# Performance work log

Hardware: AMD Instinct MI355X
Metric: run time of the kernel (lower is better)

Reference implementation:

```python
import jax, jax.numpy as jnp
import numpy as np

D = 1024
N = 16
H = D // N  # 64
F = 4096
LOG2E = 1.442695041


def _rms_norm(x, scale, eps=1e-6):
    var = jnp.mean(x * x, axis=-1, keepdims=True)
    return x * jax.lax.rsqrt(var + eps) * scale


def _layer_norm(x, gamma, beta, eps=1e-5):
    m = jnp.mean(x, axis=-1, keepdims=True)
    v = jnp.mean(jnp.square(x - m), axis=-1, keepdims=True)
    return (x - m) * jax.lax.rsqrt(v + eps) * gamma + beta


def setup_inputs() -> dict:
    key = jax.random.key(0)
    ks = jax.random.split(key, 12)
    B, T = 8, 1024
    s = 0.02
    return {
        "x": jax.random.normal(ks[0], (B, T, D), dtype=jnp.float32),
        "padding": jnp.ones((B, T), dtype=jnp.float32),
        "rms_scale": jnp.ones((D,), dtype=jnp.float32),
        "per_dim_scale": jnp.zeros((H,), dtype=jnp.float32),
        "wq": jax.random.normal(ks[1], (D, N, H), dtype=jnp.float32) * s,
        "bq": jnp.zeros((N, H), dtype=jnp.float32),
        "wk": jax.random.normal(ks[2], (D, N, H), dtype=jnp.float32) * s,
        "bk": jnp.zeros((N, H), dtype=jnp.float32),
        "wv": jax.random.normal(ks[3], (D, N, H), dtype=jnp.float32) * s,
        "bv": jnp.zeros((N, H), dtype=jnp.float32),
        "wo": jax.random.normal(ks[4], (D, N, H), dtype=jnp.float32) * s,
        "bo": jnp.zeros((D,), dtype=jnp.float32),
        "ln_gamma": jnp.ones((D,), dtype=jnp.float32),
        "ln_beta": jnp.zeros((D,), dtype=jnp.float32),
        "w1": jax.random.normal(ks[5], (D, F), dtype=jnp.float32) * s,
        "b1": jnp.zeros((F,), dtype=jnp.float32),
        "w2": jax.random.normal(ks[6], (F, D), dtype=jnp.float32) * s,
        "b2": jnp.zeros((D,), dtype=jnp.float32),
    }


def reference(x, padding, rms_scale, per_dim_scale, wq, bq, wk, bk, wv, bv,
              wo, bo, ln_gamma, ln_beta, w1, b1, w2, b2):
    B, T, _ = x.shape
    res = x
    # pre-norm (RMS) for attention block
    xn = _rms_norm(x, rms_scale)
    # causal + padding mask: [B, T, S]
    causal = jnp.tril(jnp.ones((T, T), dtype=x.dtype))
    mask = causal[None, :, :] * padding[:, :, None] * padding[:, None, :]
    # projections: [B,T,N,H]
    q = jnp.einsum("btd,dnh->btnh", xn, wq) + bq
    k = jnp.einsum("btd,dnh->btnh", xn, wk) + bk
    v = jnp.einsum("btd,dnh->btnh", xn, wv) + bv
    # per-dim scale: (log2(e)/sqrt(H)) * softplus(p)
    scale = (LOG2E / jnp.sqrt(jnp.asarray(H, x.dtype))) * jax.nn.softplus(per_dim_scale)
    q = q * scale
    # scores: [B,N,T,S]
    dot = jnp.einsum("btnh,bsnh->bnts", q, k)
    dot = jnp.where(mask[:, None, :, :] == 0, jnp.asarray(-1e9, dot.dtype), dot)
    attn_w = jax.nn.softmax(dot, axis=-1)
    attn_out = jnp.einsum("bnts,bsnh->btnh", attn_w, v)
    attn = jnp.einsum("btnh,dnh->btd", attn_out, wo) + bo
    attn = res + attn
    # FFN block (pre-norm LayerNorm)
    res2 = attn
    h = _layer_norm(attn, ln_gamma, ln_beta)
    h = jax.nn.relu(h @ w1 + b1)
    h = h @ w2 + b2
    return res2 + h
```

## Files before the change

kernel.cpp:

```cpp
#include <hip/hip_runtime.h>
#include <hip/hip_bf16.h>
#include <cstdint>
#include <cstddef>

#define BB    8
#define TT    1024
#define DD    1024
#define NHEAD 16
#define HDIM  64
#define FF    4096

typedef unsigned short u16;
typedef unsigned int   u32;
typedef short bf16x8 __attribute__((ext_vector_type(8)));
typedef float floatx4 __attribute__((ext_vector_type(4)));
typedef float floatx16 __attribute__((ext_vector_type(16)));
typedef __attribute__((address_space(1))) const u32 gu32;
typedef __attribute__((address_space(3))) u32 lu32;

#define ZERO16 {0.f,0.f,0.f,0.f,0.f,0.f,0.f,0.f,0.f,0.f,0.f,0.f,0.f,0.f,0.f,0.f}

__device__ __forceinline__ float b2f(u16 u) {
  union { u32 i; float f; } c; c.i = ((u32)u) << 16; return c.f;
}
__device__ __forceinline__ u16 f2b(float f) {
  union { float f; u32 i; } c; c.f = f;
  u32 x = c.i;
  u32 r = (x + 0x7fffu + ((x >> 16) & 1u)) >> 16;
  return (u16)r;
}

__global__ __launch_bounds__(256) void rms_kernel(const float* __restrict__ x,
                                                  const float* __restrict__ g,
                                                  u16* __restrict__ xn) {
  int row = blockIdx.x;
  int tid = threadIdx.x;
  float4 v = ((const float4*)(x + (size_t)row * DD))[tid];
  float ss = v.x*v.x + v.y*v.y + v.z*v.z + v.w*v.w;
  for (int off = 32; off; off >>= 1) ss += __shfl_xor(ss, off);
  __shared__ float red[4];
  if ((tid & 63) == 0) red[tid >> 6] = ss;
  __syncthreads();
  float tot = red[0] + red[1] + red[2] + red[3];
  float inv = rsqrtf(tot * (1.0f / DD) + 1e-6f);
  float4 gv = ((const float4*)g)[tid];
  ushort4 o;
  o.x = f2b(v.x * inv * gv.x);
  o.y = f2b(v.y * inv * gv.y);
  o.z = f2b(v.z * inv * gv.z);
  o.w = f2b(v.w * inv * gv.w);
  ((ushort4*)(xn + (size_t)row * DD))[tid] = o;
}

__global__ __launch_bounds__(256) void ln_kernel(const float* __restrict__ a,
                                                 const float* __restrict__ g,
                                                 const float* __restrict__ be,
                                                 u16* __restrict__ o) {
  int row = blockIdx.x;
  int tid = threadIdx.x;
  float4 v = ((const float4*)(a + (size_t)row * DD))[tid];
  float s1 = v.x + v.y + v.z + v.w;
  float s2 = v.x*v.x + v.y*v.y + v.z*v.z + v.w*v.w;
  for (int off = 32; off; off >>= 1) {
    s1 += __shfl_xor(s1, off);
    s2 += __shfl_xor(s2, off);
  }
  __shared__ float r1[4], r2[4];
  if ((tid & 63) == 0) { r1[tid >> 6] = s1; r2[tid >> 6] = s2; }
  __syncthreads();
  float S1 = r1[0] + r1[1] + r1[2] + r1[3];
  float S2 = r2[0] + r2[1] + r2[2] + r2[3];
  float mean = S1 * (1.0f / DD);
  float var  = S2 * (1.0f / DD) - mean * mean;
  float inv  = rsqrtf(var + 1e-5f);
  float4 gv = ((const float4*)g)[tid];
  float4 bv = ((const float4*)be)[tid];
  ushort4 out;
  out.x = f2b((v.x - mean) * inv * gv.x + bv.x);
  out.y = f2b((v.y - mean) * inv * gv.y + bv.y);
  out.z = f2b((v.z - mean) * inv * gv.z + bv.z);
  out.w = f2b((v.w - mean) * inv * gv.w + bv.w);
  ((ushort4*)(o + (size_t)row * DD))[tid] = out;
}

__global__ void prep_kernel(const float* __restrict__ bq, const float* __restrict__ bk,
                            const float* __restrict__ bv, const float* __restrict__ pds,
                            float* __restrict__ bqkv, float* __restrict__ qsall) {
  int j = blockIdx.x * 1024 + threadIdx.x;
  float b = (j < 1024) ? bq[j] : (j < 2048) ? bk[j - 1024] : bv[j - 2048];
  bqkv[j] = b;
  float s = 1.f;
  if (j < 1024) {
    float p = pds[j & 63];
    float sp = (p > 0.f) ? (p + log1pf(__expf(-p))) : log1pf(__expf(p));
    s = 0.26017112252f * sp;
  }
  qsall[j] = s;
}

__global__ __launch_bounds__(256) void transpose_conv(const float* __restrict__ in,
                                                      u16* __restrict__ out,
                                                      int R, int C) {
  __shared__ float t[32][33];
  int bx = blockIdx.x * 32, by = blockIdx.y * 32;
  int tx = threadIdx.x & 31, ty = threadIdx.x >> 5;
#pragma unroll
  for (int i = 0; i < 32; i += 8)
    t[ty + i][tx] = in[(size_t)(by + ty + i) * C + bx + tx];
  __syncthreads();
#pragma unroll
  for (int i = 0; i < 32; i += 8)
    out[(size_t)(bx + ty + i) * R + by + tx] = f2b(t[tx][ty + i]);
}

__global__ __launch_bounds__(256) void conv_bf16(const float* __restrict__ in,
                                                 u16* __restrict__ out) {
  int i = blockIdx.x * 256 + threadIdx.x;
  float4 v = ((const float4*)in)[i];
  ushort4 o = { f2b(v.x), f2b(v.y), f2b(v.z), f2b(v.w) };
  ((ushort4*)out)[i] = o;
}

__global__ __launch_bounds__(256) void vtrans_kernel(const u16* __restrict__ vsrc,
                                                     u16* __restrict__ vdst) {
  __shared__ u16 tile[64][65];
  int bn = blockIdx.y; int b = bn >> 4, n = bn & 15;
  int t0 = blockIdx.x * 64;
  int tid = threadIdx.x;
  int rr = tid >> 4;
  int c4 = (tid & 15) * 4;
#pragma unroll
  for (int i = 0; i < 4; i++) {
    int r = i * 16 + rr;
    ushort4 d = *(const ushort4*)(vsrc + ((size_t)(b * TT + t0 + r)) * DD + n * HDIM + c4);
    tile[r][c4 + 0] = d.x; tile[r][c4 + 1] = d.y;
    tile[r][c4 + 2] = d.z; tile[r][c4 + 3] = d.w;
  }
  __syncthreads();
#pragma unroll
  for (int i = 0; i < 4; i++) {
    int h = i * 16 + rr;
    ushort4 d;
    d.x = tile[c4 + 0][h]; d.y = tile[c4 + 1][h];
    d.z = tile[c4 + 2][h]; d.w = tile[c4 + 3][h];
    *(ushort4*)(vdst + ((size_t)bn * HDIM + h) * TT + t0 + c4) = d;
  }
}

template <typename OUT_T>
__global__ __launch_bounds__(512, 2) void mfma_gemm256(
    const u16* __restrict__ A, const u16* __restrict__ Bt,
    const float* __restrict__ bias, const float* __restrict__ accsrc,
    const float* __restrict__ scale, OUT_T* __restrict__ C,
    int lda, int ldb, int K, int relu, int ldc, size_t regstride) {
  __shared__ u16 As[3][256 * 32] __attribute__((aligned(16)));
  __shared__ u16 Bs[3][256 * 32] __attribute__((aligned(16)));
  int tid = threadIdx.x;
  int lane = tid & 63;
  int wv = tid >> 6;
  int nbx = gridDim.x;
  int nwg = nbx * gridDim.y;
  int bid = blockIdx.y * nbx + blockIdx.x;
  int wid = (bid & 7) * (nwg >> 3) + (bid >> 3);
  int row0 = (wid / nbx) * 256, col0 = (wid % nbx) * 256;

  int sr = tid >> 2;
  int sk = (tid & 3) << 3;
  const u16* ag = A  + (size_t)(row0 + sr) * lda + sk;
  const u16* bg = Bt + (size_t)(col0 + sr) * ldb + sk;
  size_t rstepA = (size_t)128 * lda;
  size_t rstepB = (size_t)128 * ldb;

  int fr = lane & 15, fq = lane >> 4;
  int wr = (wv >> 2) * 128;
  int wc = (wv & 3) * 64;

  floatx4 acc[8][4];
#pragma unroll
  for (int mi = 0; mi < 8; mi++)
#pragma unroll
    for (int ni = 0; ni < 4; ni++)
      acc[mi][ni] = (floatx4){0.f, 0.f, 0.f, 0.f};

#define STAGE(tt)                                                              \
  { int s_ = (tt) % 3;                                                         \
    u16* asl = As[s_] + tid * 8;                                               \
    u16* bsl = Bs[s_] + tid * 8;                                               \
    const u16* a_ = ag + (size_t)(tt) * 32;                                    \
    const u16* b_ = bg + (size_t)(tt) * 32;                                    \
    __builtin_amdgcn_global_load_lds((gu32*)a_,            (lu32*)asl,          16, 0, 0); \
    __builtin_amdgcn_global_load_lds((gu32*)(a_ + rstepA), (lu32*)(asl + 4096), 16, 0, 0); \
    __builtin_amdgcn_global_load_lds((gu32*)b_,            (lu32*)bsl,          16, 0, 0); \
    __builtin_amdgcn_global_load_lds((gu32*)(b_ + rstepB), (lu32*)(bsl + 4096), 16, 0, 0); }

  int NT = K >> 5;
  STAGE(0)
  STAGE(1)

  for (int t = 0; t < NT; ++t) {
    if (t < NT - 1) asm volatile("s_waitcnt vmcnt(4)" ::: "memory");
    else            asm volatile("s_waitcnt vmcnt(0)" ::: "memory");
    asm volatile("s_barrier" ::: "memory");
    if (t + 2 < NT) STAGE(t + 2)
    int s = t % 3;
    const u16* As_ = As[s];
    const u16* Bs_ = Bs[s];
    bf16x8 bf[4];
#pragma unroll
    for (int ni = 0; ni < 4; ni++)
      bf[ni] = *(const bf16x8*)(Bs_ + (size_t)(wc + ni * 16 + fr) * 32 + fq * 8);
    __builtin_amdgcn_s_setprio(1);
#pragma unroll
    for (int mh = 0; mh < 2; mh++) {
      bf16x8 af[4];
#pragma unroll
      for (int mi = 0; mi < 4; mi++)
        af[mi] = *(const bf16x8*)(As_ + (size_t)(wr + mh * 64 + mi * 16 + fr) * 32 + fq * 8);
#pragma unroll
      for (int mi = 0; mi < 4; mi++)
#pragma unroll
        for (int ni = 0; ni < 4; ni++)
          acc[mh * 4 + mi][ni] = __builtin_amdgcn_mfma_f32_16x16x32_bf16(
              af[mi], bf[ni], acc[mh * 4 + mi][ni], 0, 0, 0);
    }
    __builtin_amdgcn_s_setprio(0);
  }
#undef STAGE

#pragma unroll
  for (int mi = 0; mi < 8; mi++) {
    int rbase = row0 + wr + mi * 16 + fq * 4;
#pragma unroll
    for (int ni = 0; ni < 4; ni++) {
      int col = col0 + wc + ni * 16 + fr;
      float bcol = bias ? bias[col] : 0.f;
      float scl  = scale ? scale[col] : 1.f;
      size_t cbase = regstride ? ((size_t)(col >> 10) * regstride + (col & 1023))
                               : (size_t)col;
#pragma unroll
      for (int reg = 0; reg < 4; reg++) {
        int r = rbase + reg;
        float v = (acc[mi][ni][reg] + bcol) * scl;
        if (relu)   v = fmaxf(v, 0.f);
        if (accsrc) v += accsrc[(size_t)r * ldc + col];
        if constexpr (sizeof(OUT_T) == 2) ((u16*)C)[cbase + (size_t)r * ldc] = f2b(v);
        else                              ((float*)C)[cbase + (size_t)r * ldc] = v;
      }
    }
  }
}

template <typename OUT_T>
__global__ __launch_bounds__(256) void mfma_gemm(
    const u16* __restrict__ A, const u16* __restrict__ Bt,
    const float* __restrict__ bias, const float* __restrict__ accsrc,
    const float* __restrict__ scale, OUT_T* __restrict__ C,
    int lda, int ldb, int K, int relu, int ldc, size_t regstride) {
  __shared__ u16 As[2][128 * 32] __attribute__((aligned(16)));
  __shared__ u16 Bs[2][128 * 32] __attribute__((aligned(16)));
  int tid = threadIdx.x;
  int lane = tid & 63;
  int wave = tid >> 6;
  int nbx = gridDim.x;
  int nwg = nbx * gridDim.y;
  int bid = blockIdx.y * nbx + blockIdx.x;
  int wid = (bid & 7) * (nwg >> 3) + (bid >> 3);
  int row0 = (wid / nbx) * 128, col0 = (wid % nbx) * 128;

  int sr = tid >> 2;
  int sk = (tid & 3) << 3;
  const u16* ag = A  + (size_t)(row0 + sr) * lda + sk;
  const u16* bg = Bt + (size_t)(col0 + sr) * ldb + sk;
  size_t rstepA = (size_t)64 * lda;
  size_t rstepB = (size_t)64 * ldb;

  int wr = (wave >> 1) * 64;
  int wc = (wave & 1) * 64;
  int fr = lane & 15;
  int fq = lane >> 4;

  floatx4 acc[4][4];
#pragma unroll
  for (int mi = 0; mi < 4; mi++)
#pragma unroll
    for (int ni = 0; ni < 4; ni++)
      acc[mi][ni] = (floatx4){0.f, 0.f, 0.f, 0.f};

  for (int k0 = 0; k0 < K; k0 += 64) {
#pragma unroll
    for (int kk = 0; kk < 2; kk++) {
      const u16* a_ = ag + kk * 32;
      const u16* b_ = bg + kk * 32;
      u16* asl = As[kk] + tid * 8;
      u16* bsl = Bs[kk] + tid * 8;
      __builtin_amdgcn_global_load_lds((gu32*)a_,            (lu32*)asl,          16, 0, 0);
      __builtin_amdgcn_global_load_lds((gu32*)(a_ + rstepA), (lu32*)(asl + 2048), 16, 0, 0);
      __builtin_amdgcn_global_load_lds((gu32*)b_,            (lu32*)bsl,          16, 0, 0);
      __builtin_amdgcn_global_load_lds((gu32*)(b_ + rstepB), (lu32*)(bsl + 2048), 16, 0, 0);
    }
    __syncthreads();
#pragma unroll
    for (int kk = 0; kk < 2; kk++) {
      const bf16x8* afp = (const bf16x8*)(As[kk] + (size_t)(wr + fr) * 32 + fq * 8);
      const bf16x8* bfp = (const bf16x8*)(Bs[kk] + (size_t)(wc + fr) * 32 + fq * 8);
      bf16x8 af[4], bf[4];
#pragma unroll
      for (int mi = 0; mi < 4; mi++) af[mi] = afp[mi * 64];
#pragma unroll
      for (int ni = 0; ni < 4; ni++) bf[ni] = bfp[ni * 64];
#pragma unroll
      for (int mi = 0; mi < 4; mi++)
#pragma unroll
        for (int ni = 0; ni < 4; ni++)
          acc[mi][ni] = __builtin_amdgcn_mfma_f32_16x16x32_bf16(
              af[mi], bf[ni], acc[mi][ni], 0, 0, 0);
    }
    __syncthreads();
    ag += 64; bg += 64;
  }

#pragma unroll
  for (int mi = 0; mi < 4; mi++) {
    int rbase = row0 + wr + mi * 16 + fq * 4;
#pragma unroll
    for (int ni = 0; ni < 4; ni++) {
      int col = col0 + wc + ni * 16 + fr;
      float bcol = bias ? bias[col] : 0.f;
      float scl  = scale ? scale[col] : 1.f;
      size_t cbase = regstride ? ((size_t)(col >> 10) * regstride + (col & 1023))
                               : (size_t)col;
#pragma unroll
      for (int reg = 0; reg < 4; reg++) {
        int r = rbase + reg;
        float v = (acc[mi][ni][reg] + bcol) * scl;
        if (relu)   v = fmaxf(v, 0.f);
        if (accsrc) v += accsrc[(size_t)r * ldc + col];
        if constexpr (sizeof(OUT_T) == 2) ((u16*)C)[cbase + (size_t)r * ldc] = f2b(v);
        else                              ((float*)C)[cbase + (size_t)r * ldc] = v;
      }
    }
  }
}

__global__ __launch_bounds__(256) void attn_mfma(
    const u16* __restrict__ q, const u16* __restrict__ k,
    const u16* __restrict__ vT, const float* __restrict__ padc,
    u16* __restrict__ ao) {
  int nwg = gridDim.x * gridDim.y;
  int bid = blockIdx.y * gridDim.x + blockIdx.x;
  int wid = (bid & 7) * (nwg >> 3) + (bid >> 3);
  int p  = wid & 3;
  int bn = wid >> 2;
  int b = bn >> 4, n = bn & 15;
  int tid = threadIdx.x;
  int w = tid >> 6, lane = tid & 63;
  int cl = lane & 31, hf = lane >> 5;
  __shared__ u16 Qs[128 * 64] __attribute__((aligned(16)));
  __shared__ u16 Ks[64 * 64]  __attribute__((aligned(16)));
  __shared__ u16 Vts[64 * 64] __attribute__((aligned(16)));
  __shared__ float padl[64];

  for (int half = 0; half < 2; half++) {
    int qt = half ? (7 - p) : p;
    int q0g = qt * 128;

#pragma unroll
    for (int it = 0; it < 4; it++) {
      int cid = it * 256 + tid; int r = cid >> 3, cc = cid & 7;
      uint4 d = *(const uint4*)(q + ((size_t)(b * TT + q0g + r)) * DD + n * HDIM + cc * 8);
      ((uint4*)Qs)[r * 8 + (cc ^ (r & 7))] = d;
    }
    __syncthreads();
    bf16x8 qf[4];
    int qrow = 32 * w + cl;
#pragma unroll
    for (int kc = 0; kc < 4; kc++)
      qf[kc] = ((const bf16x8*)Qs)[qrow * 8 + ((2 * kc + hf) ^ (cl & 7))];

    int tq = q0g + qrow;
    float prow = padc[b * TT + tq];
    bool prow_ok = (prow != 0.f);
    floatx16 o0 = ZERO16, o1 = ZERO16;
    float m_i = -INFINITY, l_i = 0.f;

    int jend = q0g + 128;
    for (int j0 = 0; j0 < jend; j0 += 64) {
#pragma unroll
      for (int it = 0; it < 2; it++) {
        int cid = it * 256 + tid; int r = cid >> 3, cc = cid & 7;
        uint4 dk = *(const uint4*)(k + ((size_t)(b * TT + j0 + r)) * DD + n * HDIM + cc * 8);
        ((uint4*)Ks)[r * 8 + (cc ^ (r & 7))] = dk;
        uint4 dv = *(const uint4*)(vT + ((size_t)(bn * HDIM + r)) * TT + j0 + cc * 8);
        ((uint4*)Vts)[r * 8 + (cc ^ (r & 7))] = dv;
      }
      if (tid < 64) padl[tid] = padc[b * TT + j0 + tid];
      __syncthreads();

      floatx16 s0 = ZERO16, s1 = ZERO16;
#pragma unroll
      for (int kc = 0; kc < 4; kc++) {
        bf16x8 ka0 = ((const bf16x8*)Ks)[cl * 8 + ((2 * kc + hf) ^ (cl & 7))];
        bf16x8 ka1 = ((const bf16x8*)Ks)[(32 + cl) * 8 + ((2 * kc + hf) ^ (cl & 7))];
        s0 = __builtin_amdgcn_mfma_f32_32x32x16_bf16(ka0, qf[kc], s0, 0, 0, 0);
        s1 = __builtin_amdgcn_mfma_f32_32x32x16_bf16(ka1, qf[kc], s1, 0, 0, 0);
      }

      float pl = padl[lane];
      bool fullt = (j0 + 63 <= q0g + 32 * w) && __all(pl != 0.f) && __all((int)prow_ok);
      float mloc = -INFINITY;
      if (fullt) {
#pragma unroll
        for (int i = 0; i < 16; i++)
          mloc = fmaxf(mloc, fmaxf(s0[i], s1[i]));
      } else {
#pragma unroll
        for (int q2 = 0; q2 < 2; q2++) {
#pragma unroll
          for (int rg = 0; rg < 4; rg++) {
            float4 pv = *(const float4*)&padl[q2 * 32 + rg * 8 + 4 * hf];
            int kb = j0 + q2 * 32 + rg * 8 + 4 * hf;
#pragma unroll
            for (int j = 0; j < 4; j++) {
              int idx = rg * 4 + j;
              float sval = q2 ? s1[idx] : s0[idx];
              float pvj = (j == 0) ? pv.x : (j == 1) ? pv.y : (j == 2) ? pv.z : pv.w;
              bool ok = prow_ok && (kb + j <= tq) && (pvj != 0.f);
              sval = ok ? sval : -1e9f;
              if (q2) s1[idx] = sval; else s0[idx] = sval;
              mloc = fmaxf(mloc, sval);
            }
          }
        }
      }
      float mtile = fmaxf(mloc, __shfl_xor(mloc, 32));
      float mnew = fmaxf(m_i, mtile);
      float alpha = exp2f(m_i - mnew);
      m_i = mnew;
      float ls = 0.f;
#pragma unroll
      for (int i = 0; i < 16; i++) {
        float p0 = exp2f(s0[i] - mnew); s0[i] = p0; ls += p0;
        float p1 = exp2f(s1[i] - mnew); s1[i] = p1; ls += p1;
      }
      ls += __shfl_xor(ls, 32);
      l_i = l_i * alpha + ls;
      o0 *= alpha; o1 *= alpha;

      u32 pk[8][2];
#pragma unroll
      for (int q2 = 0; q2 < 2; q2++)
#pragma unroll
        for (int rg = 0; rg < 4; rg++) {
          int be = q2 * 4 + rg;
          float a0 = q2 ? s1[rg * 4 + 0] : s0[rg * 4 + 0];
          float a1 = q2 ? s1[rg * 4 + 1] : s0[rg * 4 + 1];
          float a2 = q2 ? s1[rg * 4 + 2] : s0[rg * 4 + 2];
          float a3 = q2 ? s1[rg * 4 + 3] : s0[rg * 4 + 3];
          pk[be][0] = (u32)f2b(a0) | ((u32)f2b(a1) << 16);
          pk[be][1] = (u32)f2b(a2) | ((u32)f2b(a3) << 16);
        }
      u32 pp[8][2];
#pragma unroll
      for (int be = 0; be < 8; be++) {
        pp[be][0] = (u32)__shfl_xor((int)pk[be][0], 32);
        pp[be][1] = (u32)__shfl_xor((int)pk[be][1], 32);
      }

#pragma unroll
      for (int kc = 0; kc < 4; kc++) {
        union { u32 wd[4]; bf16x8 v; } pb;
        if (hf == 0) {
          pb.wd[0] = pk[2 * kc][0];     pb.wd[1] = pk[2 * kc][1];
          pb.wd[2] = pp[2 * kc][0];     pb.wd[3] = pp[2 * kc][1];
        } else {
          pb.wd[0] = pp[2 * kc + 1][0]; pb.wd[1] = pp[2 * kc + 1][1];
          pb.wd[2] = pk[2 * kc + 1][0]; pb.wd[3] = pk[2 * kc + 1][1];
        }
        bf16x8 vf0 = ((const bf16x8*)Vts)[cl * 8 + ((2 * kc + hf) ^ (cl & 7))];
        bf16x8 vf1 = ((const bf16x8*)Vts)[(32 + cl) * 8 + ((2 * kc + hf) ^ (cl & 7))];
        o0 = __builtin_amdgcn_mfma_f32_32x32x16_bf16(vf0, pb.v, o0, 0, 0, 0);
        o1 = __builtin_amdgcn_mfma_f32_32x32x16_bf16(vf1, pb.v, o1, 0, 0, 0);
      }
      __syncthreads();
    }

    float rl = 1.f / l_i;
#pragma unroll
    for (int hq = 0; hq < 2; hq++)
#pragma unroll
      for (int rg = 0; rg < 4; rg++) {
        ushort4 st;
        st.x = f2b((hq ? o1[rg * 4 + 0] : o0[rg * 4 + 0]) * rl);
        st.y = f2b((hq ? o1[rg * 4 + 1] : o0[rg * 4 + 1]) * rl);
        st.z = f2b((hq ? o1[rg * 4 + 2] : o0[rg * 4 + 2]) * rl);
        st.w = f2b((hq ? o1[rg * 4 + 3] : o0[rg * 4 + 3]) * rl);
        int col = n * HDIM + hq * 32 + rg * 8 + 4 * hf;
        *(ushort4*)(ao + ((size_t)(b * TT + tq)) * DD + col) = st;
      }
  }
}

extern "C" void kernel_launch(void* const* d_in, const int* in_sizes, int n_in,
                              void* d_out, int out_size, void* d_ws, size_t ws_size,
                              hipStream_t stream) {
  const float* x   = (const float*)d_in[0];
  const float* pad = (const float*)d_in[1];
  const float* rs  = (const float*)d_in[2];
  const float* pds = (const float*)d_in[3];
  const float* wq  = (const float*)d_in[4];
  const float* bq  = (const float*)d_in[5];
  const float* wk  = (const float*)d_in[6];
  const float* bk  = (const float*)d_in[7];
  const float* wv_ = (const float*)d_in[8];
  const float* bv  = (const float*)d_in[9];
  const float* wo  = (const float*)d_in[10];
  const float* bo  = (const float*)d_in[11];
  const float* lg  = (const float*)d_in[12];
  const float* lb  = (const float*)d_in[13];
  const float* w1  = (const float*)d_in[14];
  const float* b1  = (const float*)d_in[15];
  const float* w2  = (const float*)d_in[16];
  const float* b2  = (const float*)d_in[17];
  float* out = (float*)d_out;

  const size_t MB = (size_t)1 << 20;
  int G;
  if      (ws_size >= 88 * MB) G = 8;
  else if (ws_size >= 56 * MB) G = 4;
  else if (ws_size >= 40 * MB) G = 2;
  else                         G = 1;

  char* w = (char*)d_ws;
  u16* wqkvT = (u16*)(w);
  u16* woT   = (u16*)(w + 6 * MB);
  u16* w1T   = (u16*)(w + 8 * MB);
  u16* w2T   = (u16*)(w + 16 * MB);
  char* act = w + 24 * MB;
  const size_t SA = (size_t)2 * G * MB;
  u16*   regA = (u16*)act;
  u16*   qB   = (u16*)(act + SA);
  u16*   kC   = (u16*)(act + 2 * SA);
  u16*   vD   = (u16*)(act + 3 * SA);
  u16*   vTr  = regA;
  u16*   ao   = vD;
  u16*   hn   = regA;
  u16*   h1h  = qB;

  float* bqkv  = out + (size_t)out_size - 8192;
  float* qsall = bqkv + 3072;

  transpose_conv<<<dim3(32, 32),  256, 0, stream>>>(wq,  wqkvT,              DD, DD);
  transpose_conv<<<dim3(32, 32),  256, 0, stream>>>(wk,  wqkvT + 1024 * 1024, DD, DD);
  transpose_conv<<<dim3(32, 32),  256, 0, stream>>>(wv_, wqkvT + 2048 * 1024, DD, DD);
  conv_bf16<<<1024, 256, 0, stream>>>(wo, woT);
  transpose_conv<<<dim3(128, 32), 256, 0, stream>>>(w1, w1T, DD, FF);
  transpose_conv<<<dim3(32, 128), 256, 0, stream>>>(w2, w2T, FF, DD);
  prep_kernel<<<3, 1024, 0, stream>>>(bq, bk, bv, pds, bqkv, qsall);

  const int R = G * 1024;

  for (int c0 = 0; c0 < BB / G; c0++) {
    size_t rowoff = (size_t)c0 * R;
    const float* xc = x + rowoff * DD;
    float* outc = out + rowoff * DD;

    rms_kernel<<<R, 256, 0, stream>>>(xc, rs, regA);

    mfma_gemm256<u16><<<dim3(12, R / 256), 512, 0, stream>>>(
        regA, wqkvT, bqkv, nullptr, qsall, qB,
        DD, DD, DD, 0, 1024, (size_t)R * 1024);

    vtrans_kernel<<<dim3(TT / 64, G * NHEAD), 256, 0, stream>>>(vD, vTr);

    attn_mfma<<<dim3(4, G * NHEAD), 256, 0, stream>>>(
        qB, kC, vTr, pad + rowoff, ao);

    mfma_gemm<float><<<dim3(8, R / 128), 256, 0, stream>>>(
        ao, woT, bo, xc, nullptr, outc, DD, DD, DD, 0, 1024, 0);

    ln_kernel<<<R, 256, 0, stream>>>(outc, lg, lb, hn);

    for (int f = 0; f < 2; f++) {
      mfma_gemm256<u16><<<dim3(8, R / 256), 512, 0, stream>>>(
          hn, w1T + (size_t)f * 2048 * 1024, b1 + f * 2048, nullptr, nullptr,
          h1h, DD, DD, DD, 1, 2048, 0);
      mfma_gemm<float><<<dim3(8, R / 128), 256, 0, stream>>>(
          h1h, w2T + f * 2048, (f == 0) ? b2 : nullptr, outc, nullptr,
          outc, 2048, FF, 2048, 0, 1024, 0);
    }
  }
}
```

Measured before the change: 618.2 us.

## Replace 256x256 triple-buffered GEMM with 128x256 four-wave synchronous-load kernel

The QKV and FFN1 GEMMs move from a 512-thread 256x256 tile with a three-stage global_load_lds pipeline to a 256-thread 128x256 tile. Each iteration loads a K=64 slice into LDS, syncs, computes, and syncs again, so loads and compute no longer overlap. Each wave now owns a 64x128 sub-tile, giving a different fragment-reuse pattern. The change trades prefetch pipelining and priority hints for a smaller LDS footprint, possibly higher occupancy and more blocks, at the risk of exposed memory latency.

```diff
diff --git a/kernel.cpp b/kernel.cpp
--- a/kernel.cpp
+++ b/kernel.cpp
@@ -148,90 +148,88 @@
 }
 
 template <typename OUT_T>
-__global__ __launch_bounds__(512, 2) void mfma_gemm256(
+__global__ __launch_bounds__(256) void mfma_gemm_wide(
     const u16* __restrict__ A, const u16* __restrict__ Bt,
     const float* __restrict__ bias, const float* __restrict__ accsrc,
     const float* __restrict__ scale, OUT_T* __restrict__ C,
     int lda, int ldb, int K, int relu, int ldc, size_t regstride) {
-  __shared__ u16 As[3][256 * 32] __attribute__((aligned(16)));
-  __shared__ u16 Bs[3][256 * 32] __attribute__((aligned(16)));
+  __shared__ u16 As[2][128 * 32] __attribute__((aligned(16)));
+  __shared__ u16 Bs[2][256 * 32] __attribute__((aligned(16)));
   int tid = threadIdx.x;
   int lane = tid & 63;
-  int wv = tid >> 6;
+  int wave = tid >> 6;
   int nbx = gridDim.x;
   int nwg = nbx * gridDim.y;
   int bid = blockIdx.y * nbx + blockIdx.x;
   int wid = (bid & 7) * (nwg >> 3) + (bid >> 3);
-  int row0 = (wid / nbx) * 256, col0 = (wid % nbx) * 256;
+  int row0 = (wid / nbx) * 128, col0 = (wid % nbx) * 256;
 
   int sr = tid >> 2;
   int sk = (tid & 3) << 3;
   const u16* ag = A  + (size_t)(row0 + sr) * lda + sk;
   const u16* bg = Bt + (size_t)(col0 + sr) * ldb + sk;
-  size_t rstepA = (size_t)128 * lda;
-  size_t rstepB = (size_t)128 * ldb;
-
-  int fr = lane & 15, fq = lane >> 4;
-  int wr = (wv >> 2) * 128;
-  int wc = (wv & 3) * 64;
-
-  floatx4 acc[8][4];
-#pragma unroll
-  for (int mi = 0; mi < 8; mi++)
-#pragma unroll
-    for (int ni = 0; ni < 4; ni++)
+  size_t rstep = (size_t)64;
+
+  int wr = (wave >> 1) * 64;
+  int wc = (wave & 1) * 128;
+  int fr = lane & 15;
+  int fq = lane >> 4;
+
+  floatx4 acc[4][8];
+#pragma unroll
+  for (int mi = 0; mi < 4; mi++)
+#pragma unroll
+    for (int ni = 0; ni < 8; ni++)
       acc[mi][ni] = (floatx4){0.f, 0.f, 0.f, 0.f};
 
-#define STAGE(tt)                                                              \
-  { int s_ = (tt) % 3;                                                         \
-    u16* asl = As[s_] + tid * 8;                                               \
-    u16* bsl = Bs[s_] + tid * 8;                                               \
-    const u16* a_ = ag + (size_t)(tt) * 32;                                    \
-    const u16* b_ = bg + (size_t)(tt) * 32;                                    \
-    __builtin_amdgcn_global_load_lds((gu32*)a_,            (lu32*)asl,          16, 0, 0); \
-    __builtin_amdgcn_global_load_lds((gu32*)(a_ + rstepA), (lu32*)(asl + 4096), 16, 0, 0); \
-    __builtin_amdgcn_global_load_lds((gu32*)b_,            (lu32*)bsl,          16, 0, 0); \
-    __builtin_amdgcn_global_load_lds((gu32*)(b_ + rstepB), (lu32*)(bsl + 4096), 16, 0, 0); }
-
-  int NT = K >> 5;
-  STAGE(0)
-  STAGE(1)
-
-  for (int t = 0; t < NT; ++t) {
-    if (t < NT - 1) asm volatile("s_waitcnt vmcnt(4)" ::: "memory");
-    else            asm volatile("s_waitcnt vmcnt(0)" ::: "memory");
-    asm volatile("s_barrier" ::: "memory");
-    if (t + 2 < NT) STAGE(t + 2)
-    int s = t % 3;
-    const u16* As_ = As[s];
-    const u16* Bs_ = Bs[s];
-    bf16x8 bf[4];
-#pragma unroll
-    for (int ni = 0; ni < 4; ni++)
-      bf[ni] = *(const bf16x8*)(Bs_ + (size_t)(wc + ni * 16 + fr) * 32 + fq * 8);
-    __builtin_amdgcn_s_setprio(1);
-#pragma unroll
-    for (int mh = 0; mh < 2; mh++) {
-      bf16x8 af[4];
+  for (int k0 = 0; k0 < K; k0 += 64) {
+#pragma unroll
+    for (int kk = 0; kk < 2; kk++) {
+      const u16* a_ = ag + kk * 32;
+      const u16* b_ = bg + kk * 32;
+      u16* asl = As[kk] + tid * 8;
+      u16* bsl = Bs[kk] + tid * 8;
+      __builtin_amdgcn_global_load_lds((gu32*)a_,                  (lu32*)asl,          16, 0, 0);
+      __builtin_amdgcn_global_load_lds((gu32*)(a_ + rstep * lda),  (lu32*)(asl + 2048), 16, 0, 0);
+      __builtin_amdgcn_global_load_lds((gu32*)b_,                  (lu32*)bsl,          16, 0, 0);
+      __builtin_amdgcn_global_load_lds((gu32*)(b_ + rstep * ldb),      (lu32*)(bsl + 2048), 16, 0, 0);
+      __builtin_amdgcn_global_load_lds((gu32*)(b_ + 2 * rstep * ldb),  (lu32*)(bsl + 4096), 16, 0, 0);
+      __builtin_amdgcn_global_load_lds((gu32*)(b_ + 3 * rstep * ldb),  (lu32*)(bsl + 6144), 16, 0, 0);
+    }
+    __syncthreads();
+#pragma unroll
+    for (int kk = 0; kk < 2; kk++) {
+      const bf16x8* afp = (const bf16x8*)(As[kk] + (size_t)(wr + fr) * 32 + fq * 8);
+      const bf16x8* bfp = (const bf16x8*)(Bs[kk] + (size_t)(wc + fr) * 32 + fq * 8);
+      bf16x8 af[4], bf[4];
+#pragma unroll
+      for (int mi = 0; mi < 4; mi++) af[mi] = afp[mi * 64];
+#pragma unroll
+      for (int ni = 0; ni < 4; ni++) bf[ni] = bfp[ni * 64];
 #pragma unroll
       for (int mi = 0; mi < 4; mi++)
-        af[mi] = *(const bf16x8*)(As_ + (size_t)(wr + mh * 64 + mi * 16 + fr) * 32 + fq * 8);
+#pragma unroll
+        for (int ni = 0; ni < 4; ni++)
+          acc[mi][ni] = __builtin_amdgcn_mfma_f32_16x16x32_bf16(
+              af[mi], bf[ni], acc[mi][ni], 0, 0, 0);
+#pragma unroll
+      for (int ni = 0; ni < 4; ni++) bf[ni] = bfp[(ni + 4) * 64];
 #pragma unroll
       for (int mi = 0; mi < 4; mi++)
 #pragma unroll
         for (int ni = 0; ni < 4; ni++)
-          acc[mh * 4 + mi][ni] = __builtin_amdgcn_mfma_f32_16x16x32_bf16(
-              af[mi], bf[ni], acc[mh * 4 + mi][ni], 0, 0, 0);
-    }
-    __builtin_amdgcn_s_setprio(0);
-  }
-#undef STAGE
-
-#pragma unroll
-  for (int mi = 0; mi < 8; mi++) {
+          acc[mi][ni + 4] = __builtin_amdgcn_mfma_f32_16x16x32_bf16(
+              af[mi], bf[ni], acc[mi][ni + 4], 0, 0, 0);
+    }
+    __syncthreads();
+    ag += 64; bg += 64;
+  }
+
+#pragma unroll
+  for (int mi = 0; mi < 4; mi++) {
     int rbase = row0 + wr + mi * 16 + fq * 4;
 #pragma unroll
-    for (int ni = 0; ni < 4; ni++) {
+    for (int ni = 0; ni < 8; ni++) {
       int col = col0 + wc + ni * 16 + fr;
       float bcol = bias ? bias[col] : 0.f;
       float scl  = scale ? scale[col] : 1.f;
@@ -566,7 +564,7 @@
 
     rms_kernel<<<R, 256, 0, stream>>>(xc, rs, regA);
 
-    mfma_gemm256<u16><<<dim3(12, R / 256), 512, 0, stream>>>(
+    mfma_gemm_wide<u16><<<dim3(12, R / 128), 256, 0, stream>>>(
         regA, wqkvT, bqkv, nullptr, qsall, qB,
         DD, DD, DD, 0, 1024, (size_t)R * 1024);
 
@@ -581,7 +579,7 @@
     ln_kernel<<<R, 256, 0, stream>>>(outc, lg, lb, hn);
 
     for (int f = 0; f < 2; f++) {
-      mfma_gemm256<u16><<<dim3(8, R / 256), 512, 0, stream>>>(
+      mfma_gemm_wide<u16><<<dim3(8, R / 128), 256, 0, stream>>>(
           hn, w1T + (size_t)f * 2048 * 1024, b1 + f * 2048, nullptr, nullptr,
           h1h, DD, DD, DD, 1, 2048, 0);
       mfma_gemm<float><<<dim3(8, R / 128), 256, 0, stream>>>(
```

Measured after the change: 704.7 us. +14.0%, slower.
